# Performance work log

Hardware: AMD Instinct MI355X
Metric: run time of the kernel (lower is better)

## Reference

```python
import jax, jax.numpy as jnp
import numpy as np

B, N, T, N_IN = 8, 64, 128, 8
N_EMB = 64
E = N * (N - 1)  # fully connected, no self loops


def _rel_matrices():
    off_diag = np.ones((N, N), dtype=np.float32) - np.eye(N, dtype=np.float32)
    recv_idx, send_idx = np.where(off_diag)
    rel_rec = np.eye(N, dtype=np.float32)[recv_idx]   # [E, N]
    rel_send = np.eye(N, dtype=np.float32)[send_idx]  # [E, N]
    return jnp.asarray(rel_rec), jnp.asarray(rel_send)


def setup_inputs() -> dict:
    key = jax.random.key(0)
    ks = jax.random.split(key, 8)
    x = jax.random.normal(ks[0], (B, N, T, N_IN), dtype=jnp.float32)
    rel_rec, rel_send = _rel_matrices()
    s = lambda fan_in: 1.0 / np.sqrt(fan_in)
    W_sp = jax.random.uniform(ks[1], (3 * N_IN, N_EMB), minval=-s(3 * N_IN), maxval=s(3 * N_IN))
    b_sp = jax.random.uniform(ks[2], (N_EMB,), minval=-s(3 * N_IN), maxval=s(3 * N_IN))
    W_node = jax.random.uniform(ks[3], (N_IN, N_EMB), minval=-s(N_IN), maxval=s(N_IN))
    b_node = jax.random.uniform(ks[4], (N_EMB,), minval=-s(N_IN), maxval=s(N_IN))
    W_att = jax.random.uniform(ks[5], (N_EMB, 1), minval=-s(N_EMB), maxval=s(N_EMB))
    b_att = jax.random.uniform(ks[6], (1,), minval=-s(N_EMB), maxval=s(N_EMB))
    return {"x": x, "rel_rec": rel_rec, "rel_send": rel_send,
            "W_sp": W_sp, "b_sp": b_sp, "W_node": W_node, "b_node": b_node,
            "W_att": W_att, "b_att": b_att}


def reference(x, rel_rec, rel_send, W_sp, b_sp, W_node, b_node, W_att, b_att):
    lrelu = jax.nn.leaky_relu  # slope 0.01, matches F.leaky_relu default

    # gather senders per edge: [B, E, T, F]
    senders = jnp.einsum('en,bntf->betf', rel_send, x)
    # NOTE: faithful to source bug: receivers = senders.view(...) overwrites
    receivers = senders
    spatial_relations = receivers - senders  # zeros, as in the original

    nodes_embed = x @ W_node + b_node  # [B, N, T, D]

    # model_increment=True branch
    xd = x[:, :, 1:, :] - x[:, :, :-1, :]  # [B, N, T-1, F]
    senders = jnp.einsum('en,bntf->betf', rel_send, xd)
    receivers = senders  # same bug replicated
    rec_send = jnp.concatenate([senders, receivers], axis=-1)  # [B, E, T-1, 2F]
    spatial_relations = jnp.concatenate(
        [spatial_relations[:, :, :-1, :], rec_send], axis=-1)  # [B, E, T-1, 3F]
    nodes_embed = nodes_embed[:, :, :-1, :]  # [B, N, T-1, D]

    spatial_embed = spatial_relations @ W_sp + b_sp  # [B, E, T-1, D]

    nodes_embed = jnp.transpose(nodes_embed, (0, 2, 1, 3))    # [B, T-1, N, D]
    spatial_embed = jnp.transpose(spatial_embed, (0, 2, 1, 3))  # [B, T-1, E, D]

    receivers_embed = jnp.einsum('en,btnd->bted', rel_rec, nodes_embed)
    senders_embed = jnp.einsum('en,btnd->bted', rel_send, nodes_embed)
    agg = receivers_embed + senders_embed + spatial_embed  # [B, T-1, E, D]

    attention = lrelu((agg @ W_att + b_att)[..., 0])  # [B, T-1, E]
    # rel_rec.T @ diag(attention) @ rel_send, without materializing [E, E]
    A = jnp.einsum('en,bte,ef->btnf', rel_rec, attention, rel_send)  # [B,T-1,N,N]
    A = jax.nn.softmax(A, axis=-1)
    return lrelu(A @ nodes_embed)  # [B, T-1, N, D]
```

## Files before the change

### kernel.cpp

```cpp
#include <hip/hip_runtime.h>
#include <math.h>

#define BB 8
#define TM1 127

typedef _Float16 f16x4 __attribute__((ext_vector_type(4)));
typedef float f32x4 __attribute__((ext_vector_type(4)));
typedef unsigned int u32x4 __attribute__((ext_vector_type(4)));

__device__ __forceinline__ float lrelu(float v) { return v > 0.0f ? v : 0.01f * v; }

__global__ __launch_bounds__(256, 4) void gat_kernel(
    const float* __restrict__ x,
    const float* __restrict__ W_sp,
    const float* __restrict__ b_sp,
    const float* __restrict__ W_node,
    const float* __restrict__ b_node,
    const float* __restrict__ W_att,
    const float* __restrict__ b_att,
    float* __restrict__ out)
{
    const int bt = blockIdx.x;
    const int b = bt / TM1;
    const int t = bt - b * TM1;
    const int tid = threadIdx.x;
    const int lane = tid & 63;
    const int wid = tid >> 6;

    __shared__ __align__(16) float x2[2][64][8];
    __shared__ __align__(16) unsigned short Nh[64][72];
    __shared__ __align__(16) float u_sh[64];
    __shared__ __align__(16) float w_sh[64];

    {
        int n = tid >> 2;
        int sel = tid & 3;
        int tile = sel >> 1, half = sel & 1;
        const float* src = x + (((long)(b * 64 + n) * 128) + (t + tile)) * 8 + half * 4;
        *(float4*)&x2[tile][n][half * 4] = *(const float4*)src;
    }
    float Wn[8];
#pragma unroll
    for (int k = 0; k < 8; ++k) Wn[k] = W_node[k * 64 + lane];
    const float bnode_d = b_node[lane];
    const float batt = b_att[0];

    float pv[8], qv[8], c0, c1;
    {
        float wa = W_att[lane];
        float vals[18];
#pragma unroll
        for (int k = 0; k < 8; ++k) vals[k] = Wn[k] * wa;
#pragma unroll
        for (int k = 0; k < 8; ++k)
            vals[8 + k] = (W_sp[(8 + k) * 64 + lane] + W_sp[(16 + k) * 64 + lane]) * wa;
        vals[16] = b_sp[lane] * wa;
        vals[17] = bnode_d * wa;
#pragma unroll
        for (int i = 0; i < 18; ++i) {
            float v = vals[i];
#pragma unroll
            for (int off = 32; off > 0; off >>= 1) v += __shfl_xor(v, off, 64);
            vals[i] = v;
        }
#pragma unroll
        for (int k = 0; k < 8; ++k) { pv[k] = vals[k]; qv[k] = vals[8 + k]; }
        c0 = vals[16]; c1 = vals[17];
    }
    __syncthreads();

    if (tid < 64) {
        f32x4 a0 = *(const f32x4*)&x2[0][tid][0];
        f32x4 a1 = *(const f32x4*)&x2[0][tid][4];
        f32x4 d0 = *(const f32x4*)&x2[1][tid][0];
        f32x4 d1 = *(const f32x4*)&x2[1][tid][4];
        float su = 0.f, sw = 0.f;
#pragma unroll
        for (int e = 0; e < 4; ++e) {
            su += a0[e] * pv[e] + a1[e] * pv[4 + e];
            sw += (d0[e] - a0[e]) * qv[e] + (d1[e] - a1[e]) * qv[4 + e];
        }
        u_sh[tid] = su + c1;
        w_sh[tid] = sw + c0;
    }

    {
        unsigned int hw[8];
#pragma unroll
        for (int p = 0; p < 8; ++p) {
            float acc0 = bnode_d, acc1 = bnode_d;
            int f0 = wid * 16 + 2 * p;
            f32x4 xa = *(const f32x4*)&x2[0][f0][0];
            f32x4 xb = *(const f32x4*)&x2[0][f0][4];
            f32x4 ya = *(const f32x4*)&x2[0][f0 + 1][0];
            f32x4 yb = *(const f32x4*)&x2[0][f0 + 1][4];
#pragma unroll
            for (int e = 0; e < 4; ++e) {
                acc0 += xa[e] * Wn[e] + xb[e] * Wn[4 + e];
                acc1 += ya[e] * Wn[e] + yb[e] * Wn[4 + e];
            }
            _Float16 h0 = (_Float16)acc0, h1 = (_Float16)acc1;
            hw[p] = (unsigned int)__builtin_bit_cast(unsigned short, h0) |
                    ((unsigned int)__builtin_bit_cast(unsigned short, h1) << 16);
        }
        u32x4 qa = {hw[0], hw[1], hw[2], hw[3]};
        u32x4 qb = {hw[4], hw[5], hw[6], hw[7]};
        *(u32x4*)&Nh[lane][wid * 16]     = qa;
        *(u32x4*)&Nh[lane][wid * 16 + 8] = qb;
    }
    __syncthreads();

    {
        const int i = lane & 15;
        const int g4 = (lane >> 4) * 4;
        const int n = wid * 16 + i;
        const float un = u_sh[n];

        float a[16];
#pragma unroll
        for (int s4 = 0; s4 < 4; ++s4) {
            f32x4 uf = *(const f32x4*)&u_sh[s4 * 16 + g4];
            f32x4 wf = *(const f32x4*)&w_sh[s4 * 16 + g4];
#pragma unroll
            for (int e = 0; e < 4; ++e) {
                int f = s4 * 16 + g4 + e;
                float v = lrelu(un + uf[e] + wf[e] + batt);
                a[s4 * 4 + e] = (f == n) ? 0.0f : v;
            }
        }
        float m = a[0];
#pragma unroll
        for (int j = 1; j < 16; ++j) m = fmaxf(m, a[j]);
        m = fmaxf(m, __shfl_xor(m, 16, 64));
        m = fmaxf(m, __shfl_xor(m, 32, 64));
        float s = 0.f;
#pragma unroll
        for (int j = 0; j < 16; ++j) {
            float e = __expf(a[j] - m);
            a[j] = e;
            s += e;
        }
        s += __shfl_xor(s, 16, 64);
        s += __shfl_xor(s, 32, 64);
        const float inv = 1.0f / s;

        f16x4 Ah[4];
#pragma unroll
        for (int s4 = 0; s4 < 4; ++s4)
#pragma unroll
            for (int e = 0; e < 4; ++e)
                Ah[s4][e] = (_Float16)(a[s4 * 4 + e] * inv);

        f32x4 acc[4];
#pragma unroll
        for (int c = 0; c < 4; ++c) acc[c] = (f32x4){0.f, 0.f, 0.f, 0.f};

#pragma unroll
        for (int c = 0; c < 4; ++c) {
            const int col = c * 16 + i;
#pragma unroll
            for (int s4 = 0; s4 < 4; ++s4) {
                f16x4 bh = *(const f16x4*)&Nh[col][s4 * 16 + g4];
                acc[c] = __builtin_amdgcn_mfma_f32_16x16x16f16(Ah[s4], bh, acc[c], 0, 0, 0);
            }
        }

        float* op = out + ((long)(b * TM1 + t) << 12);
#pragma unroll
        for (int c = 0; c < 4; ++c) {
#pragma unroll
            for (int r = 0; r < 4; ++r) {
                int row = wid * 16 + g4 + r;
                op[row * 64 + c * 16 + i] = lrelu(acc[c][r]);
            }
        }
    }
}

extern "C" void kernel_launch(void* const* d_in, const int* in_sizes, int n_in,
                              void* d_out, int out_size, void* d_ws, size_t ws_size,
                              hipStream_t stream) {
    const float* x      = (const float*)d_in[0];
    const float* W_sp   = (const float*)d_in[3];
    const float* b_sp   = (const float*)d_in[4];
    const float* W_node = (const float*)d_in[5];
    const float* b_node = (const float*)d_in[6];
    const float* W_att  = (const float*)d_in[7];
    const float* b_att  = (const float*)d_in[8];
    float* out = (float*)d_out;

    dim3 grid(BB * TM1);
    dim3 block(256);
    hipLaunchKernelGGL(gat_kernel, grid, block, 0, stream,
                       x, W_sp, b_sp, W_node, b_node, W_att, b_att, out);
}
```

Baseline: 17.55 us.

## Split attention-vector reductions across waves and load x directly from global

The 18 wave-wide butterfly reductions that every wave previously repeated are now divided so each wave reduces about five of them, and the results are shared through a small LDS array. The x staging buffer in LDS is removed. Node embeddings read x rows through wave-uniform (readfirstlane) scalar addresses, and wave 0 keeps its own x rows in registers to compute u/w after a barrier. This cuts redundant shuffle work and the initial LDS fill. The cost is an extra barrier and more global/scalar loads.

```diff
diff --git a/kernel.cpp b/kernel.cpp
--- a/kernel.cpp
+++ b/kernel.cpp
@@ -27,77 +27,70 @@
     const int lane = tid & 63;
     const int wid = tid >> 6;
 
-    __shared__ __align__(16) float x2[2][64][8];
     __shared__ __align__(16) unsigned short Nh[64][72];
     __shared__ __align__(16) float u_sh[64];
     __shared__ __align__(16) float w_sh[64];
-
-    {
-        int n = tid >> 2;
-        int sel = tid & 3;
-        int tile = sel >> 1, half = sel & 1;
-        const float* src = x + (((long)(b * 64 + n) * 128) + (t + tile)) * 8 + half * 4;
-        *(float4*)&x2[tile][n][half * 4] = *(const float4*)src;
-    }
+    __shared__ __align__(16) float red[20];
+
+    const float wa = W_att[lane];
     float Wn[8];
 #pragma unroll
     for (int k = 0; k < 8; ++k) Wn[k] = W_node[k * 64 + lane];
     const float bnode_d = b_node[lane];
     const float batt = b_att[0];
 
-    float pv[8], qv[8], c0, c1;
+    f32x4 xa0, xa1, xd0, xd1;
+    if (wid == 0) {
+        const float* xr = x + ((b * 64 + lane) * 128 + t) * 8;
+        xa0 = *(const f32x4*)(xr);
+        xa1 = *(const f32x4*)(xr + 4);
+        xd0 = *(const f32x4*)(xr + 8);
+        xd1 = *(const f32x4*)(xr + 12);
+    }
+
     {
-        float wa = W_att[lane];
-        float vals[18];
-#pragma unroll
-        for (int k = 0; k < 8; ++k) vals[k] = Wn[k] * wa;
-#pragma unroll
-        for (int k = 0; k < 8; ++k)
-            vals[8 + k] = (W_sp[(8 + k) * 64 + lane] + W_sp[(16 + k) * 64 + lane]) * wa;
-        vals[16] = b_sp[lane] * wa;
-        vals[17] = bnode_d * wa;
-#pragma unroll
-        for (int i = 0; i < 18; ++i) {
-            float v = vals[i];
-#pragma unroll
-            for (int off = 32; off > 0; off >>= 1) v += __shfl_xor(v, off, 64);
-            vals[i] = v;
-        }
-#pragma unroll
-        for (int k = 0; k < 8; ++k) { pv[k] = vals[k]; qv[k] = vals[8 + k]; }
-        c0 = vals[16]; c1 = vals[17];
-    }
-    __syncthreads();
-
-    if (tid < 64) {
-        f32x4 a0 = *(const f32x4*)&x2[0][tid][0];
-        f32x4 a1 = *(const f32x4*)&x2[0][tid][4];
-        f32x4 d0 = *(const f32x4*)&x2[1][tid][0];
-        f32x4 d1 = *(const f32x4*)&x2[1][tid][4];
-        float su = 0.f, sw = 0.f;
-#pragma unroll
-        for (int e = 0; e < 4; ++e) {
-            su += a0[e] * pv[e] + a1[e] * pv[4 + e];
-            sw += (d0[e] - a0[e]) * qv[e] + (d1[e] - a1[e]) * qv[4 + e];
-        }
-        u_sh[tid] = su + c1;
-        w_sh[tid] = sw + c0;
+        const int v0 = wid * 5;
+        float pr[5];
+#pragma unroll
+        for (int j = 0; j < 5; ++j) {
+            int v = v0 + j;
+            float val;
+            if (v < 8)       val = W_node[v * 64 + lane] * wa;
+            else if (v < 16) val = (W_sp[v * 64 + lane] + W_sp[(v + 8) * 64 + lane]) * wa;
+            else if (v == 16) val = b_sp[lane] * wa;
+            else             val = bnode_d * wa;
+            pr[j] = val;
+        }
+#pragma unroll
+        for (int j = 0; j < 5; ++j) {
+            float vv = pr[j];
+#pragma unroll
+            for (int off = 1; off < 64; off <<= 1) vv += __shfl_xor(vv, off, 64);
+            pr[j] = vv;
+        }
+        if (lane == 0) {
+#pragma unroll
+            for (int j = 0; j < 5; ++j) {
+                int v = v0 + j;
+                if (v < 18) red[v] = pr[j];
+            }
+        }
     }
 
     {
         unsigned int hw[8];
 #pragma unroll
         for (int p = 0; p < 8; ++p) {
+            int f0 = wid * 16 + 2 * p;
+            int off = ((b * 64 + f0) * 128 + t) * 8;
+            off = __builtin_amdgcn_readfirstlane(off);
+            const float* r0 = x + off;
+            const float* r1 = r0 + 1024;
             float acc0 = bnode_d, acc1 = bnode_d;
-            int f0 = wid * 16 + 2 * p;
-            f32x4 xa = *(const f32x4*)&x2[0][f0][0];
-            f32x4 xb = *(const f32x4*)&x2[0][f0][4];
-            f32x4 ya = *(const f32x4*)&x2[0][f0 + 1][0];
-            f32x4 yb = *(const f32x4*)&x2[0][f0 + 1][4];
-#pragma unroll
-            for (int e = 0; e < 4; ++e) {
-                acc0 += xa[e] * Wn[e] + xb[e] * Wn[4 + e];
-                acc1 += ya[e] * Wn[e] + yb[e] * Wn[4 + e];
+#pragma unroll
+            for (int e = 0; e < 8; ++e) {
+                acc0 += r0[e] * Wn[e];
+                acc1 += r1[e] * Wn[e];
             }
             _Float16 h0 = (_Float16)acc0, h1 = (_Float16)acc1;
             hw[p] = (unsigned int)__builtin_bit_cast(unsigned short, h0) |
@@ -107,6 +100,18 @@
         u32x4 qb = {hw[4], hw[5], hw[6], hw[7]};
         *(u32x4*)&Nh[lane][wid * 16]     = qa;
         *(u32x4*)&Nh[lane][wid * 16 + 8] = qb;
+    }
+    __syncthreads();
+
+    if (wid == 0) {
+        float su = 0.f, sw = 0.f;
+#pragma unroll
+        for (int e = 0; e < 4; ++e) {
+            su += xa0[e] * red[e] + xa1[e] * red[4 + e];
+            sw += (xd0[e] - xa0[e]) * red[8 + e] + (xd1[e] - xa1[e]) * red[12 + e];
+        }
+        u_sh[lane] = su + red[17];
+        w_sh[lane] = sw + red[16];
     }
     __syncthreads();
 
```

Measured after the change: 14.69 us. 16.3% less time.
